# Kernel tuning notes

Hardware: AMD Instinct MI355X
Metric: run time of the kernel (lower is better)

## Reference

```python
import jax, jax.numpy as jnp
import numpy as np

EMBED_DIM = 1024
TASK_BIAS_DIM = 128
BATCH = 4
SEQ = 2048


def setup_inputs() -> dict:
    key = jax.random.key(0)
    kq, kk, kv, kt, kw, kb = jax.random.split(key, 6)
    query = jax.random.normal(kq, (BATCH, SEQ, EMBED_DIM), dtype=jnp.float32)
    key_t = jax.random.normal(kk, (BATCH, SEQ, EMBED_DIM), dtype=jnp.float32)
    value = jax.random.normal(kv, (BATCH, SEQ, EMBED_DIM), dtype=jnp.float32)
    task_bias = jax.random.normal(kt, (BATCH, TASK_BIAS_DIM), dtype=jnp.float32)
    # task_bias_proj: Linear(task_bias_dim, 1) -> weight [1, task_bias_dim], bias [1]
    lim = 1.0 / np.sqrt(TASK_BIAS_DIM)
    W = jax.random.uniform(kw, (TASK_BIAS_DIM, 1), jnp.float32, -lim, lim)
    b = jax.random.uniform(kb, (1,), jnp.float32, -lim, lim)
    return {"query": query, "key": key_t, "value": value,
            "task_bias": task_bias, "W": W, "b": b}


def reference(query, key, value, task_bias, W, b):
    scale = EMBED_DIM ** 0.5
    # scores: [batch, seq, seq]
    scores = jnp.einsum('bqd,bkd->bqk', query, key) / scale
    # per-batch scalar gate from task bias: [batch, 1]
    gate = jax.nn.sigmoid(task_bias @ W + b)           # [batch, 1]
    scores = scores * gate[:, :, None]                 # broadcast [b,1,1]
    attention_weights = jax.nn.softmax(scores, axis=-1)
    output = jnp.einsum('bqk,bkd->bqd', attention_weights, value)
    return output, attention_weights
```

## Files before the change

### kernel.cpp

```cpp
#include <hip/hip_runtime.h>
#include <hip/hip_bf16.h>
#include <stdint.h>
#include <stddef.h>

#define B_  4
#define S_  2048
#define D_  1024
#define TB_ 128

typedef float v4f  __attribute__((ext_vector_type(4)));
typedef short s16x4 __attribute__((ext_vector_type(4)));
typedef short s16x8 __attribute__((ext_vector_type(8)));

#define WAITV(n) asm volatile("s_waitcnt vmcnt(" #n ")" ::: "memory")

__device__ __forceinline__ unsigned short f2bf(float f) {
  union { float f; unsigned u; } x; x.f = f;
  unsigned u = x.u;
  unsigned r = (u + 0x7FFFu + ((u >> 16) & 1u)) >> 16;
  return (unsigned short)r;
}

__device__ __forceinline__ void gld16(const void* g, void* l) {
  __builtin_amdgcn_global_load_lds(
      (const __attribute__((address_space(1))) unsigned int*)g,
      (__attribute__((address_space(3))) unsigned int*)l, 16, 0, 0);
}

__device__ __forceinline__ void barrier_sync() {
  asm volatile("" ::: "memory");
  __builtin_amdgcn_s_barrier();
  asm volatile("" ::: "memory");
  __builtin_amdgcn_sched_barrier(0);
}

__global__ __launch_bounds__(256) void prep_kernel(
    const float* __restrict__ Q, const float* __restrict__ K,
    const float* __restrict__ V, const float* __restrict__ tb,
    const float* __restrict__ W, const float* __restrict__ bias,
    short* __restrict__ Qb, short* __restrict__ Kb,
    short* __restrict__ VT, float* __restrict__ gate) {
  __shared__ float tile[64][65];
  int bid = blockIdx.x;
  int t = threadIdx.x;
  if (bid < 16384) {
    const float* src = bid < 8192 ? Q : K;
    short* dst = bid < 8192 ? Qb : Kb;
    size_t g = (size_t)(bid & 8191) * 256 + t;
    v4f v = *(const v4f*)(src + g * 4);
    s16x4 o;
    o[0] = (short)f2bf(v[0]); o[1] = (short)f2bf(v[1]);
    o[2] = (short)f2bf(v[2]); o[3] = (short)f2bf(v[3]);
    *(s16x4*)(dst + g * 4) = o;
  } else if (bid < 18432) {
    int v = bid - 16384;
    int b = v >> 9;
    int rem = v & 511;
    int s0 = (rem & 31) * 64, d0 = (rem >> 5) * 64;
    int tc = t & 63, tr4 = t >> 6;
    const float* src = V + ((size_t)b * S_ + s0) * D_ + d0;
    #pragma unroll
    for (int p = 0; p < 16; ++p) {
      int r = p * 4 + tr4;
      tile[r][tc] = src[(size_t)r * D_ + tc];
    }
    __syncthreads();
    short* dst = VT + ((size_t)b * D_ + d0) * S_ + s0;
    #pragma unroll
    for (int p = 0; p < 16; ++p) {
      int r = p * 4 + tr4;
      dst[(size_t)r * S_ + tc] = (short)f2bf(tile[tc][r]);
    }
  } else {
    int b = t >> 6, l = t & 63;
    float s = tb[b * TB_ + l] * W[l] + tb[b * TB_ + 64 + l] * W[64 + l];
    #pragma unroll
    for (int off = 32; off > 0; off >>= 1) s += __shfl_down(s, off, 64);
    if (l == 0) gate[b] = 1.0f / (1.0f + __expf(-(s + bias[0])));
  }
}

template<int MTILES, int NTILES, int KT, int BROWS, int LDC, bool GATED>
__global__ __launch_bounds__(512, 1) void gemm_coh(
    const short* __restrict__ Ag, const short* __restrict__ Bg,
    const float* __restrict__ gate, float* __restrict__ Cg) {
  extern __shared__ char lds[];
  constexpr int NT = KT / 64;
  constexpr int PB = MTILES * NTILES;
  constexpr int CPX = (4 * PB) / 8;
  constexpr int ABYTES = 256 * 128;
  constexpr int BUFB = ABYTES + 128 * 128;

  int wg = blockIdx.x;
  int swz = (wg & 7) * CPX + (wg >> 3);
  int b = swz / PB;
  int rem = swz % PB;
  int m0 = (rem / NTILES) * 256;
  int n0 = (rem % NTILES) * 128;

  int tid = threadIdx.x;
  int w = tid >> 6, l = tid & 63;
  int wm = w >> 1, wn = w & 1;
  int l7 = l & 7, fr = l & 15, hi = l >> 4;

  const short* Ab = Ag + (size_t)b * S_ * KT + (size_t)m0 * KT;
  const short* Bb = Bg + (size_t)b * BROWS * KT + (size_t)n0 * KT;

  int srow8 = l >> 3;
  int schunk = (l7 ^ srow8) * 8;

  v4f acc[4][4];
  #pragma unroll
  for (int m = 0; m < 4; ++m)
    #pragma unroll
    for (int n = 0; n < 4; ++n)
      #pragma unroll
      for (int j = 0; j < 4; ++j) acc[m][n][j] = 0.0f;

  auto stage = [&](int t, int buf) {
    char* La = lds + buf * BUFB;
    char* Lb = La + ABYTES;
    const short* As = Ab + (size_t)t * 64 + schunk;
    const short* Bs = Bb + (size_t)t * 64 + schunk;
    #pragma unroll
    for (int j = 0; j < 4; ++j) {
      int blk = w * 4 + j;
      gld16(As + (size_t)(blk * 8 + srow8) * KT, La + blk * 1024);
    }
    #pragma unroll
    for (int j = 0; j < 2; ++j) {
      int blk = w * 2 + j;
      gld16(Bs + (size_t)(blk * 8 + srow8) * KT, Lb + blk * 1024);
    }
  };

  stage(0, 0);
  int cur = 0;
  for (int t = 0; t < NT; ++t) {
    if (t + 1 < NT) {
      stage(t + 1, cur ^ 1);
      WAITV(6);
    } else {
      WAITV(0);
    }
    barrier_sync();
    const char* Abase = lds + cur * BUFB;
    const char* Bbase = Abase + ABYTES;
    #pragma unroll
    for (int kk = 0; kk < 2; ++kk) {
      int slot = ((kk * 4 + hi) ^ l7) * 16;
      s16x8 af[4], bfr[4];
      #pragma unroll
      for (int m = 0; m < 4; ++m)
        af[m] = *(const s16x8*)(Abase +
                 (size_t)(wm * 64 + m * 16 + fr) * 128 + slot);
      #pragma unroll
      for (int n = 0; n < 4; ++n)
        bfr[n] = *(const s16x8*)(Bbase +
                 (size_t)(wn * 64 + n * 16 + fr) * 128 + slot);
      __builtin_amdgcn_s_setprio(1);
      #pragma unroll
      for (int m = 0; m < 4; ++m)
        #pragma unroll
        for (int n = 0; n < 4; ++n)
          acc[m][n] = __builtin_amdgcn_mfma_f32_16x16x32_bf16(
              af[m], bfr[n], acc[m][n], 0, 0, 0);
      __builtin_amdgcn_s_setprio(0);
    }
    barrier_sync();
    cur ^= 1;
  }

  float g = 1.0f;
  if constexpr (GATED) g = gate[b] * 0.03125f;
  float* Cb = Cg + (size_t)b * S_ * LDC +
              (size_t)(m0 + wm * 64) * LDC + n0 + wn * 64;
  #pragma unroll
  for (int mf = 0; mf < 4; ++mf)
    #pragma unroll
    for (int nf = 0; nf < 4; ++nf) {
      int r0 = mf * 16 + hi * 4;
      int c = nf * 16 + fr;
      #pragma unroll
      for (int j = 0; j < 4; ++j)
        Cb[(size_t)(r0 + j) * LDC + c] = acc[mf][nf][j] * g;
    }
}

__global__ __launch_bounds__(256) void softmax_kernel(
    float* __restrict__ attn, short* __restrict__ attnb) {
  size_t row = blockIdx.x;
  float* p = attn + row * S_;
  int t = threadIdx.x;
  v4f v0 = *(const v4f*)(p + t * 8);
  v4f v1 = *(const v4f*)(p + t * 8 + 4);
  float m = fmaxf(fmaxf(fmaxf(v0[0], v0[1]), fmaxf(v0[2], v0[3])),
                  fmaxf(fmaxf(v1[0], v1[1]), fmaxf(v1[2], v1[3])));
  #pragma unroll
  for (int off = 32; off > 0; off >>= 1) m = fmaxf(m, __shfl_xor(m, off, 64));
  __shared__ float rm[4], rs[4];
  if ((t & 63) == 0) rm[t >> 6] = m;
  __syncthreads();
  m = fmaxf(fmaxf(rm[0], rm[1]), fmaxf(rm[2], rm[3]));
  float e[8]; float sum = 0.0f;
  #pragma unroll
  for (int j = 0; j < 4; ++j) { e[j] = __expf(v0[j] - m); sum += e[j]; }
  #pragma unroll
  for (int j = 0; j < 4; ++j) { e[4 + j] = __expf(v1[j] - m); sum += e[4 + j]; }
  #pragma unroll
  for (int off = 32; off > 0; off >>= 1) sum += __shfl_xor(sum, off, 64);
  if ((t & 63) == 0) rs[t >> 6] = sum;
  __syncthreads();
  sum = rs[0] + rs[1] + rs[2] + rs[3];
  float inv = 1.0f / sum;
  #pragma unroll
  for (int j = 0; j < 4; ++j) v0[j] = e[j] * inv;
  #pragma unroll
  for (int j = 0; j < 4; ++j) v1[j] = e[4 + j] * inv;
  *(v4f*)(p + t * 8) = v0;
  *(v4f*)(p + t * 8 + 4) = v1;
  s16x8 ob;
  ob[0] = (short)f2bf(v0[0]); ob[1] = (short)f2bf(v0[1]);
  ob[2] = (short)f2bf(v0[2]); ob[3] = (short)f2bf(v0[3]);
  ob[4] = (short)f2bf(v1[0]); ob[5] = (short)f2bf(v1[1]);
  ob[6] = (short)f2bf(v1[2]); ob[7] = (short)f2bf(v1[3]);
  *(s16x8*)(attnb + row * S_ + t * 8) = ob;
}

extern "C" void kernel_launch(void* const* d_in, const int* in_sizes, int n_in,
                              void* d_out, int out_size, void* d_ws, size_t ws_size,
                              hipStream_t stream) {
  (void)in_sizes; (void)n_in; (void)out_size; (void)ws_size;
  const float* Q  = (const float*)d_in[0];
  const float* K  = (const float*)d_in[1];
  const float* V  = (const float*)d_in[2];
  const float* tb = (const float*)d_in[3];
  const float* W  = (const float*)d_in[4];
  const float* bias = (const float*)d_in[5];

  float* out  = (float*)d_out;
  float* attn = out + (size_t)B_ * S_ * D_;

  char* ws = (char*)d_ws;
  float* gate = (float*)ws;
  short* Qb = (short*)(ws + 256);
  short* Kb = Qb + (size_t)B_ * S_ * D_;
  short* VT = Kb + (size_t)B_ * S_ * D_;
  short* attnb = Qb;

  auto* qkf = gemm_coh<8, 16, 1024, 2048, 2048, true>;
  auto* pvf = gemm_coh<8, 8, 2048, 1024, 1024, false>;
  constexpr int G_LDS = 2 * (256 + 128) * 64 * 2;
  (void)hipFuncSetAttribute((const void*)qkf,
      hipFuncAttributeMaxDynamicSharedMemorySize, G_LDS);
  (void)hipFuncSetAttribute((const void*)pvf,
      hipFuncAttributeMaxDynamicSharedMemorySize, G_LDS);

  prep_kernel<<<18433, 256, 0, stream>>>(Q, K, V, tb, W, bias,
                                         Qb, Kb, VT, gate);
  qkf<<<512, 512, G_LDS, stream>>>(Qb, Kb, gate, attn);
  softmax_kernel<<<8192, 256, 0, stream>>>(attn, attnb);
  pvf<<<256, 512, G_LDS, stream>>>(attnb, VT, gate, out);
}
```

Baseline: 139.2 us.

## Replace double-buffered GEMM with triple-buffer ring and per-quarter staged loads

Rewrites the bf16 MFMA GEMM mainloop as a three-slot LDS ring with a prefetch depth of two k-tiles. Global-to-LDS loads are split into thirds and interleaved across four per-row-fragment sub-steps, each separated by barriers. The aim is to hide global load latency and spread LDS traffic across the compute. In exchange it adds more barriers per k-tile and raises LDS use to 144 KB, which limits residency to one workgroup per CU.

Measured after the change: 142.4 us. 2.4% more time.

```diff
diff --git a/kernel.cpp b/kernel.cpp
--- a/kernel.cpp
+++ b/kernel.cpp
@@ -80,23 +80,22 @@
   }
 }
 
-template<int MTILES, int NTILES, int KT, int BROWS, int LDC, bool GATED>
-__global__ __launch_bounds__(512, 1) void gemm_coh(
+template<int TN, int KT, int BROWS, int LDC, bool GATED>
+__global__ __launch_bounds__(512, 1) void gemm_ring(
     const short* __restrict__ Ag, const short* __restrict__ Bg,
     const float* __restrict__ gate, float* __restrict__ Cg) {
   extern __shared__ char lds[];
-  constexpr int NT = KT / 64;
-  constexpr int PB = MTILES * NTILES;
+  constexpr int NKT = KT / 64;
+  constexpr int BUFB = 3 * 16384;
+  constexpr int PB = 8 * TN;
   constexpr int CPX = (4 * PB) / 8;
-  constexpr int ABYTES = 256 * 128;
-  constexpr int BUFB = ABYTES + 128 * 128;
 
   int wg = blockIdx.x;
   int swz = (wg & 7) * CPX + (wg >> 3);
   int b = swz / PB;
   int rem = swz % PB;
-  int m0 = (rem / NTILES) * 256;
-  int n0 = (rem % NTILES) * 128;
+  int m0 = (rem / TN) * 256;
+  int n0 = (rem % TN) * 128;
 
   int tid = threadIdx.x;
   int w = tid >> 6, l = tid & 63;
@@ -106,8 +105,17 @@
   const short* Ab = Ag + (size_t)b * S_ * KT + (size_t)m0 * KT;
   const short* Bb = Bg + (size_t)b * BROWS * KT + (size_t)n0 * KT;
 
-  int srow8 = l >> 3;
-  int schunk = (l7 ^ srow8) * 8;
+  int schunk = ((tid & 7) ^ ((tid >> 3) & 7)) * 8;
+
+  auto stage_half = [&](int tt, int h, int tgtbuf) {
+    char* base = lds + tgtbuf * BUFB + h * 16384;
+    const short* src = (h < 2)
+        ? (Ab + (size_t)(h * 128 + (tid >> 3)) * KT)
+        : (Bb + (size_t)(tid >> 3) * KT);
+    src += (size_t)tt * 64 + schunk;
+    gld16(src, base + tid * 16);
+    gld16(src + (size_t)64 * KT, base + 8192 + tid * 16);
+  };
 
   v4f acc[4][4];
   #pragma unroll
@@ -117,58 +125,56 @@
       #pragma unroll
       for (int j = 0; j < 4; ++j) acc[m][n][j] = 0.0f;
 
-  auto stage = [&](int t, int buf) {
-    char* La = lds + buf * BUFB;
-    char* Lb = La + ABYTES;
-    const short* As = Ab + (size_t)t * 64 + schunk;
-    const short* Bs = Bb + (size_t)t * 64 + schunk;
-    #pragma unroll
-    for (int j = 0; j < 4; ++j) {
-      int blk = w * 4 + j;
-      gld16(As + (size_t)(blk * 8 + srow8) * KT, La + blk * 1024);
-    }
-    #pragma unroll
-    for (int j = 0; j < 2; ++j) {
-      int blk = w * 2 + j;
-      gld16(Bs + (size_t)(blk * 8 + srow8) * KT, Lb + blk * 1024);
-    }
-  };
-
-  stage(0, 0);
-  int cur = 0;
-  for (int t = 0; t < NT; ++t) {
-    if (t + 1 < NT) {
-      stage(t + 1, cur ^ 1);
-      WAITV(6);
-    } else {
-      WAITV(0);
-    }
-    barrier_sync();
-    const char* Abase = lds + cur * BUFB;
-    const char* Bbase = Abase + ABYTES;
-    #pragma unroll
-    for (int kk = 0; kk < 2; ++kk) {
-      int slot = ((kk * 4 + hi) ^ l7) * 16;
-      s16x8 af[4], bfr[4];
-      #pragma unroll
-      for (int m = 0; m < 4; ++m)
-        af[m] = *(const s16x8*)(Abase +
-                 (size_t)(wm * 64 + m * 16 + fr) * 128 + slot);
-      #pragma unroll
-      for (int n = 0; n < 4; ++n)
-        bfr[n] = *(const s16x8*)(Bbase +
-                 (size_t)(wn * 64 + n * 16 + fr) * 128 + slot);
+  #pragma unroll
+  for (int tt = 0; tt < 2; ++tt)
+    #pragma unroll
+    for (int h = 0; h < 3; ++h) stage_half(tt, h, tt);
+  WAITV(6);
+  barrier_sync();
+
+  int bufc = 0;
+  for (int kt = 0; kt < NKT; ++kt) {
+    const char* bb = lds + bufc * BUFB;
+    int tgt = bufc + 2; if (tgt >= 3) tgt -= 3;
+    bool stage_on = (kt < NKT - 2);
+    s16x8 bf[4][2];
+    #pragma unroll
+    for (int q = 0; q < 4; ++q) {
+      if (q == 0) {
+        #pragma unroll
+        for (int nf = 0; nf < 4; ++nf) {
+          int rb = wn * 64 + nf * 16 + fr;
+          const char* rp = bb + 32768 + (size_t)rb * 128;
+          bf[nf][0] = *(const s16x8*)(rp + ((0 + hi) ^ l7) * 16);
+          bf[nf][1] = *(const s16x8*)(rp + ((4 + hi) ^ l7) * 16);
+        }
+      }
+      s16x8 af[2];
+      {
+        int ra = wm * 64 + q * 16 + fr;
+        const char* rp = bb + (ra >> 7) * 16384 + (size_t)(ra & 127) * 128;
+        af[0] = *(const s16x8*)(rp + ((0 + hi) ^ l7) * 16);
+        af[1] = *(const s16x8*)(rp + ((4 + hi) ^ l7) * 16);
+      }
+      if (stage_on && q < 3) stage_half(kt + 2, q, tgt);
+      if (q == 3) {
+        if (kt < NKT - 2) { WAITV(6); } else { WAITV(0); }
+      }
+      barrier_sync();
+      asm volatile("s_waitcnt lgkmcnt(0)" ::: "memory");
+      __builtin_amdgcn_sched_barrier(0);
       __builtin_amdgcn_s_setprio(1);
       #pragma unroll
-      for (int m = 0; m < 4; ++m)
-        #pragma unroll
-        for (int n = 0; n < 4; ++n)
-          acc[m][n] = __builtin_amdgcn_mfma_f32_16x16x32_bf16(
-              af[m], bfr[n], acc[m][n], 0, 0, 0);
+      for (int nf = 0; nf < 4; ++nf) {
+        acc[q][nf] = __builtin_amdgcn_mfma_f32_16x16x32_bf16(
+            af[0], bf[nf][0], acc[q][nf], 0, 0, 0);
+        acc[q][nf] = __builtin_amdgcn_mfma_f32_16x16x32_bf16(
+            af[1], bf[nf][1], acc[q][nf], 0, 0, 0);
+      }
       __builtin_amdgcn_s_setprio(0);
-    }
-    barrier_sync();
-    cur ^= 1;
+      barrier_sync();
+    }
+    if (++bufc == 3) bufc = 0;
   }
 
   float g = 1.0f;
@@ -248,9 +254,9 @@
   short* VT = Kb + (size_t)B_ * S_ * D_;
   short* attnb = Qb;
 
-  auto* qkf = gemm_coh<8, 16, 1024, 2048, 2048, true>;
-  auto* pvf = gemm_coh<8, 8, 2048, 1024, 1024, false>;
-  constexpr int G_LDS = 2 * (256 + 128) * 64 * 2;
+  auto* qkf = gemm_ring<16, 1024, 2048, 2048, true>;
+  auto* pvf = gemm_ring<8, 2048, 1024, 1024, false>;
+  constexpr int G_LDS = 3 * 3 * 16384;
   (void)hipFuncSetAttribute((const void*)qkf,
       hipFuncAttributeMaxDynamicSharedMemorySize, G_LDS);
   (void)hipFuncSetAttribute((const void*)pvf,
```
